# Performance work log

Hardware: AMD Instinct MI355X
Metric: run time of the kernel (lower is better)

The kernel has to match this reference:

```python
import jax, jax.numpy as jnp
import numpy as np

B, CIN, COUT, K, H, W, STYLE_DIM = 16, 128, 128, 3, 128, 128, 512

def setup_inputs() -> dict:
    key = jax.random.key(0)
    k1, k2, k3, k4 = jax.random.split(key, 4)
    x = jax.random.normal(k1, (B, CIN, H, W), dtype=jnp.float32)
    style = jax.random.normal(k2, (B, STYLE_DIM), dtype=jnp.float32)
    weight = jax.random.normal(k3, (COUT, CIN, K, K), dtype=jnp.float32)
    mod_w = jax.random.normal(k4, (CIN, STYLE_DIM), dtype=jnp.float32)
    mod_b = jnp.ones((CIN,), dtype=jnp.float32)  # EqualLinear bias_init=1
    return {"x": x, "style": style, "weight": weight, "mod_w": mod_w, "mod_b": mod_b}

def reference(x, style, weight, mod_w, mod_b):
    b, cin, h, w = x.shape
    cout, _, k, _ = weight.shape
    scale = 1.0 / np.sqrt(cin * k * k)        # conv equalized-lr scale
    lin_scale = 1.0 / np.sqrt(mod_w.shape[1])  # EqualLinear scale (lr_mul=1)
    pad = k // 2
    # affine modulation: EqualLinear(style_dim -> in_channels), bias_init=1
    s = style @ (mod_w * lin_scale).T + mod_b               # [B, Cin]
    # per-sample modulated weights
    wmod = scale * weight[None] * s[:, None, :, None, None]  # [B, Cout, Cin, k, k]
    demod = jax.lax.rsqrt(jnp.sum(wmod * wmod, axis=(2, 3, 4)) + 1e-8)  # [B, Cout]
    wmod = wmod * demod[:, :, None, None, None]
    # grouped conv with groups=batch == vmapped per-sample conv
    def conv_one(xi, wi):
        return jax.lax.conv_general_dilated(
            xi[None], wi, window_strides=(1, 1), padding=[(pad, pad), (pad, pad)],
            dimension_numbers=("NCHW", "OIHW", "NCHW"))[0]
    out = jax.vmap(conv_one)(x, wmod)  # [B, Cout, H, W]
    return out
```

## Files before the change

### kernel.cpp

```cpp
#include <hip/hip_runtime.h>
#include <hip/hip_bf16.h>


typedef __attribute__((ext_vector_type(8))) short short8;
typedef __attribute__((ext_vector_type(4))) float f32x4;

#define CONV_SCALE 0.029462782549439483f
#define LIN_SCALE 0.04419417382415922f

__device__ __forceinline__ void async16(unsigned short* lds, const unsigned short* g) {
  __builtin_amdgcn_global_load_lds((const __attribute__((address_space(1))) void*)g,
                                   (__attribute__((address_space(3))) void*)lds, 16, 0, 0);
}

__device__ __forceinline__ unsigned int pack2bf(float a, float b) {
  unsigned short ha = __builtin_bit_cast(unsigned short, __float2bfloat16(a));
  unsigned short hb = __builtin_bit_cast(unsigned short, __float2bfloat16(b));
  return (unsigned int)ha | ((unsigned int)hb << 16);
}

__global__ void style_kernel(const float* __restrict__ style, const float* __restrict__ mod_w,
                             const float* __restrict__ mod_b, float* __restrict__ s_ws) {
  const int gw = blockIdx.x * 4 + (threadIdx.x >> 6);
  const int b = gw >> 7, cin = gw & 127, lane = threadIdx.x & 63;
  const float4 s0 = *(const float4*)(style + (size_t)b * 512 + lane * 4);
  const float4 s1 = *(const float4*)(style + (size_t)b * 512 + 256 + lane * 4);
  const float4 w0 = *(const float4*)(mod_w + (size_t)cin * 512 + lane * 4);
  const float4 w1 = *(const float4*)(mod_w + (size_t)cin * 512 + 256 + lane * 4);
  float acc = s0.x * w0.x + s0.y * w0.y + s0.z * w0.z + s0.w * w0.w +
              s1.x * w1.x + s1.y * w1.y + s1.z * w1.z + s1.w * w1.w;
#pragma unroll
  for (int off = 32; off; off >>= 1) acc += __shfl_xor(acc, off);
  if (lane == 0) s_ws[b * 128 + cin] = acc * LIN_SCALE + mod_b[cin];
}

__global__ void modw_kernel(const float* __restrict__ weight, const float* __restrict__ s_ws,
                            unsigned short* __restrict__ w_ws) {
  const int bid = blockIdx.x;
  const int b = bid >> 7, cout = bid & 127;
  const int cin = threadIdx.x;
  const float sv = s_ws[b * 128 + cin] * CONV_SCALE;
  const float* wp = weight + ((size_t)cout * 128 + cin) * 9;
  float v[9];
  float ss = 0.f;
#pragma unroll
  for (int j = 0; j < 9; ++j) { v[j] = wp[j] * sv; ss += v[j] * v[j]; }
#pragma unroll
  for (int off = 32; off; off >>= 1) ss += __shfl_down(ss, off);
  __shared__ float red[2];
  if ((threadIdx.x & 63) == 0) red[threadIdx.x >> 6] = ss;
  __syncthreads();
  const float dem = rsqrtf(red[0] + red[1] + 1e-8f);
#pragma unroll
  for (int j = 0; j < 9; ++j) {
    __hip_bfloat16 h = __float2bfloat16(v[j] * dem);
    w_ws[(((size_t)b * 9 + j) * 128 + cout) * 128 + cin] =
        __builtin_bit_cast(unsigned short, h);
  }
}

__device__ __forceinline__ void transpose_row(const float* __restrict__ xb, int c0, int yy,
                                              unsigned short* __restrict__ dst, int tid) {
  const int tcq = tid & 15, t4 = tid >> 4;
  if (yy < 0 || yy > 127) {
    const uint2 z = {0u, 0u};
#pragma unroll
    for (int xi = 0; xi < 2; ++xi)
#pragma unroll
      for (int i = 0; i < 4; ++i) {
        const int xp = (xi * 16 + t4) * 4 + i;
        *(uint2*)(dst + xp * 64 + (((tcq >> 1) ^ (xp & 7)) << 3) + ((tcq & 1) << 2)) = z;
      }
    return;
  }
  const float* row = xb + (size_t)(c0 + tcq * 4) * 16384 + (size_t)yy * 128;
#pragma unroll
  for (int xi = 0; xi < 2; ++xi) {
    const int xq = xi * 16 + t4;
    float4 f[4];
#pragma unroll
    for (int j = 0; j < 4; ++j) f[j] = *(const float4*)(row + (size_t)j * 16384 + xq * 4);
#pragma unroll
    for (int i = 0; i < 4; ++i) {
      const int xp = xq * 4 + i;
      uint2 col;
      col.x = pack2bf(((const float*)&f[0])[i], ((const float*)&f[1])[i]);
      col.y = pack2bf(((const float*)&f[2])[i], ((const float*)&f[3])[i]);
      *(uint2*)(dst + xp * 64 + (((tcq >> 1) ^ (xp & 7)) << 3) + ((tcq & 1) << 2)) = col;
    }
  }
}

__global__ __launch_bounds__(256, 3) void conv_kernel(const float* __restrict__ x,
                                                      const unsigned short* __restrict__ wws,
                                                      float* __restrict__ out) {
  __shared__ unsigned short xr[2 * 128 * 64];
  __shared__ unsigned short lA[128 * 64];

  const int tid = threadIdx.x;
  const int bid = (blockIdx.x & 7) * 256 + (blockIdx.x >> 3);
  const int b = bid >> 7, y = bid & 127;
  const int lane = tid & 63, w = tid >> 6;
  const int wm = w & 1, wn = w >> 1;
  const int l15 = lane & 15, q = lane >> 4;

  f32x4 acc[4][4];
#pragma unroll
  for (int i = 0; i < 4; ++i)
#pragma unroll
    for (int t = 0; t < 4; ++t) acc[i][t] = (f32x4){0.f, 0.f, 0.f, 0.f};

  const float* xb = x + (size_t)b * (128 * 16384);
  const unsigned short* wb = wws + (size_t)b * 9 * 128 * 128;

  const int mbase = tid >> 3;
  const int goff = (((tid & 7) ^ ((tid >> 3) & 7)) << 3);
  const int eoff = tid * 8;

  int nt[4];
#pragma unroll
  for (int t = 0; t < 4; ++t) nt[t] = wn * 64 + t * 16 + l15;

  const short8 zero8 = {0, 0, 0, 0, 0, 0, 0, 0};

  for (int c0 = 0; c0 < 128; c0 += 64) {
    __syncthreads();
    transpose_row(xb, c0, y - 1, xr, tid);
    transpose_row(xb, c0, y, xr + 8192, tid);
    for (int ky = 0; ky < 3; ++ky) {
      for (int kx = 0; kx < 3; ++kx) {
        const int j3 = ky * 3 + kx;
        if (j3) __syncthreads();
#pragma unroll
        for (int p = 0; p < 4; ++p)
          async16(lA + p * 2048 + eoff, wb + j3 * 16384 + c0 + p * 4096 + mbase * 128 + goff);
        if (ky == 1 && kx == 0) transpose_row(xb, c0, y + 1, xr, tid);
        __syncthreads();
        const unsigned short* xkr = xr + ((ky & 1) << 13);
        int xcb[4];
#pragma unroll
        for (int t = 0; t < 4; ++t) xcb[t] = nt[t] + (kx - 1);
        const bool lo = (xcb[0] < 0);
        const bool hi = (xcb[3] > 127);
        if (lo) xcb[0] = 0;
        if (hi) xcb[3] = 127;
#pragma unroll
        for (int s = 0; s < 2; ++s) {
          const int s4q = s * 4 + q;
          const int axor = ((s4q ^ (l15 & 7)) << 3);
          short8 af[4], bf[4];
#pragma unroll
          for (int i = 0; i < 4; ++i)
            af[i] = *(const short8*)(lA + (wm * 64 + i * 16 + l15) * 64 + axor);
#pragma unroll
          for (int t = 0; t < 4; ++t)
            bf[t] = *(const short8*)(xkr + xcb[t] * 64 + ((s4q ^ (xcb[t] & 7)) << 3));
          if (lo) bf[0] = zero8;
          if (hi) bf[3] = zero8;
#pragma unroll
          for (int i = 0; i < 4; ++i)
#pragma unroll
            for (int t = 0; t < 4; ++t)
              acc[i][t] = __builtin_amdgcn_mfma_f32_16x16x32_bf16(af[i], bf[t], acc[i][t], 0, 0, 0);
        }
      }
    }
  }

  float* ob = out + ((size_t)b * 128 * 128 + y) * 128;
#pragma unroll
  for (int i = 0; i < 4; ++i) {
    const int coutb = wm * 64 + i * 16 + q * 4;
#pragma unroll
    for (int rr = 0; rr < 4; ++rr) {
      float* orow = ob + (size_t)(coutb + rr) * (128 * 128);
#pragma unroll
      for (int t = 0; t < 4; ++t) orow[wn * 64 + t * 16 + l15] = acc[i][t][rr];
    }
  }
}

extern "C" void kernel_launch(void* const* d_in, const int* in_sizes, int n_in,
                              void* d_out, int out_size, void* d_ws, size_t ws_size,
                              hipStream_t stream) {
  const float* x = (const float*)d_in[0];
  const float* style = (const float*)d_in[1];
  const float* weight = (const float*)d_in[2];
  const float* mod_w = (const float*)d_in[3];
  const float* mod_b = (const float*)d_in[4];
  float* out = (float*)d_out;

  char* ws = (char*)d_ws;
  float* s_ws = (float*)ws;
  unsigned short* w_ws = (unsigned short*)(ws + 8192);

  style_kernel<<<512, 256, 0, stream>>>(style, mod_w, mod_b, s_ws);
  modw_kernel<<<16 * 128, 128, 0, stream>>>(weight, s_ws, w_ws);
  conv_kernel<<<16 * 128, 256, 0, stream>>>(x, w_ws, out);
}
```

Before: 307.9 us.

## Double-buffer modulated-weight tiles and reload a single input row per ky

The conv kernel now double-buffers the per-tap weight tile in LDS. It prefetches the next (c0, ky, kx) tile asynchronously while MFMAs run on the current one, and uses one barrier per tap instead of two. To keep LDS usage the same, the two-row input buffer becomes a single row that is transposed and refilled at the start of each ky. The aim is to hide weight-load latency and cut barriers. In exchange, the input-row transpose is no longer overlapped with compute and sits directly on the critical path.

```diff
diff --git a/kernel.cpp b/kernel.cpp
--- a/kernel.cpp
+++ b/kernel.cpp
@@ -94,8 +94,8 @@
 __global__ __launch_bounds__(256, 3) void conv_kernel(const float* __restrict__ x,
                                                       const unsigned short* __restrict__ wws,
                                                       float* __restrict__ out) {
-  __shared__ unsigned short xr[2 * 128 * 64];
-  __shared__ unsigned short lA[128 * 64];
+  __shared__ unsigned short xr[128 * 64];
+  __shared__ unsigned short lA[2][128 * 64];
 
   const int tid = threadIdx.x;
   const int bid = (blockIdx.x & 7) * 256 + (blockIdx.x >> 3);
@@ -123,20 +123,29 @@
 
   const short8 zero8 = {0, 0, 0, 0, 0, 0, 0, 0};
 
-  for (int c0 = 0; c0 < 128; c0 += 64) {
-    __syncthreads();
-    transpose_row(xb, c0, y - 1, xr, tid);
-    transpose_row(xb, c0, y, xr + 8192, tid);
+#pragma unroll
+  for (int p = 0; p < 4; ++p)
+    async16(lA[0] + p * 2048 + eoff, wb + p * 4096 + mbase * 128 + goff);
+
+  int par = 0;
+  for (int h = 0; h < 2; ++h) {
+    const int c0 = h << 6;
     for (int ky = 0; ky < 3; ++ky) {
+      transpose_row(xb, c0, y + ky - 1, xr, tid);
+      __syncthreads();
       for (int kx = 0; kx < 3; ++kx) {
-        const int j3 = ky * 3 + kx;
-        if (j3) __syncthreads();
-#pragma unroll
-        for (int p = 0; p < 4; ++p)
-          async16(lA + p * 2048 + eoff, wb + j3 * 16384 + c0 + p * 4096 + mbase * 128 + goff);
-        if (ky == 1 && kx == 0) transpose_row(xb, c0, y + 1, xr, tid);
-        __syncthreads();
-        const unsigned short* xkr = xr + ((ky & 1) << 13);
+        const bool last = (h == 1) && (ky == 2) && (kx == 2);
+        if (!last) {
+          const int nkx = (kx < 2) ? kx + 1 : 0;
+          const int nky = (kx < 2) ? ky : ((ky < 2) ? ky + 1 : 0);
+          const int nc0 = (kx == 2 && ky == 2) ? 64 : c0;
+          const int nj3 = nky * 3 + nkx;
+          unsigned short* dst = lA[par ^ 1];
+#pragma unroll
+          for (int p = 0; p < 4; ++p)
+            async16(dst + p * 2048 + eoff, wb + nj3 * 16384 + nc0 + p * 4096 + mbase * 128 + goff);
+        }
+        const unsigned short* Ab = lA[par];
         int xcb[4];
 #pragma unroll
         for (int t = 0; t < 4; ++t) xcb[t] = nt[t] + (kx - 1);
@@ -151,10 +160,10 @@
           short8 af[4], bf[4];
 #pragma unroll
           for (int i = 0; i < 4; ++i)
-            af[i] = *(const short8*)(lA + (wm * 64 + i * 16 + l15) * 64 + axor);
+            af[i] = *(const short8*)(Ab + (wm * 64 + i * 16 + l15) * 64 + axor);
 #pragma unroll
           for (int t = 0; t < 4; ++t)
-            bf[t] = *(const short8*)(xkr + xcb[t] * 64 + ((s4q ^ (xcb[t] & 7)) << 3));
+            bf[t] = *(const short8*)(xr + xcb[t] * 64 + ((s4q ^ (xcb[t] & 7)) << 3));
           if (lo) bf[0] = zero8;
           if (hi) bf[3] = zero8;
 #pragma unroll
@@ -163,6 +172,8 @@
             for (int t = 0; t < 4; ++t)
               acc[i][t] = __builtin_amdgcn_mfma_f32_16x16x32_bf16(af[i], bf[t], acc[i][t], 0, 0, 0);
         }
+        __syncthreads();
+        par ^= 1;
       }
     }
   }
```

New measurement: 323.2 us. 1.05x slower.
